# Optimization experiments

Hardware: AMD Instinct MI355X
Metric: run time of the kernel (lower is better)

Reference implementation:

```python
import jax, jax.numpy as jnp
import numpy as np

K = 4  # hard-coded in ParticleNet.__init__

# (fan_in, fan_out) for all linear layers
_DIMS = [(10, 32), (32, 64),        # edgeconv1 MLP (2*5 -> 32 -> 64)
         (128, 96), (96, 128),      # edgeconv2 MLP (2*64 -> 96 -> 128)
         (256, 192), (192, 256),    # edgeconv3 MLP (2*128 -> 192 -> 256)
         (453, 453), (453, 226), (226, 2)]  # output head (5+64+128+256=453)
_PNAMES = ['c1w1', 'c1w2', 'c2w1', 'c2w2', 'c3w1', 'c3w2', 'ow1', 'ow2', 'ow3']


def setup_inputs() -> dict:
    key = jax.random.key(0)
    ks = jax.random.split(key, 2 + len(_DIMS))
    inp = {
        'coords': jax.random.normal(ks[0], (1024, 128, 2), dtype=jnp.float32),
        'features': jax.random.normal(ks[1], (1024, 128, 5), dtype=jnp.float32),
    }
    for i, (name, (fi, fo)) in enumerate(zip(_PNAMES, _DIMS)):
        inp[name] = jax.random.normal(ks[2 + i], (fi, fo), dtype=jnp.float32) / np.sqrt(fi)
        inp[name.replace('w', 'b')] = jnp.zeros((fo,), dtype=jnp.float32)
    return inp


def _knn_idx(x, k):
    # x: [B,N,C] -> idx of k nearest neighbors (excluding self): [B,N,k]
    x2 = jnp.sum(x * x, axis=-1)                              # [B,N]
    d = x2[:, :, None] + x2[:, None, :] - 2.0 * jnp.einsum('bnc,bmc->bnm', x, x)
    d = d + jnp.eye(x.shape[1], dtype=x.dtype) * 1e9          # no self-loops
    _, idx = jax.lax.top_k(-d, k)
    return idx


def _edgeconv(x, idx, w1, b1, w2, b2):
    # EdgeConv: message = MLP([x_i, x_j - x_i]), mean-aggregated over k neighbors
    xj = jax.vmap(lambda xb, ib: xb[ib])(x, idx)              # [B,N,k,C]
    xi = jnp.broadcast_to(x[:, :, None, :], xj.shape)
    h = jnp.concatenate([xi, xj - xi], axis=-1)               # [B,N,k,2C]
    h = jax.nn.elu(h @ w1 + b1)
    h = jax.nn.elu(h @ w2 + b2)
    return jnp.mean(h, axis=2)                                # [B,N,out]


def reference(coords, features, c1w1, c1b1, c1w2, c1b2, c2w1, c2b1, c2w2, c2b2,
              c3w1, c3b1, c3w2, c3b2, ow1, ob1, ow2, ob2, ow3, ob3):
    idx1 = _knn_idx(coords, K)
    out1 = _edgeconv(features, idx1, c1w1, c1b1, c1w2, c1b2)  # [B,N,64]
    idx2 = _knn_idx(out1, K)
    out2 = _edgeconv(out1, idx2, c2w1, c2b1, c2w2, c2b2)      # [B,N,128]
    idx3 = _knn_idx(out2, K)
    out3 = _edgeconv(out2, idx3, c3w1, c3b1, c3w2, c3b2)      # [B,N,256]
    h = jnp.concatenate([features, out1, out2, out3], axis=-1)  # [B,N,453]
    h = jax.nn.elu(h @ ow1 + ob1)
    h = jax.nn.elu(h @ ow2 + ob2)
    return h @ ow3 + ob3                                      # [B,N,2]
```

## Files before the change

kernel.cpp:

```cpp
#include <hip/hip_runtime.h>
#include <cstdint>
#include <cstddef>


#define NB 1024
#define NPT 128

typedef __attribute__((ext_vector_type(8))) short short8;
typedef __attribute__((ext_vector_type(4))) float floatx4;
typedef __attribute__((ext_vector_type(4))) unsigned int uint4v;

__device__ __forceinline__ float elu_f(float x) { return x > 0.0f ? x : expm1f(x); }

__device__ __forceinline__ unsigned short f2bf(float f) {
  unsigned u = __builtin_bit_cast(unsigned, f);
  unsigned r = u + 0x7FFFu + ((u >> 16) & 1u);
  return (unsigned short)(r >> 16);
}
__device__ __forceinline__ float bf2f(unsigned short h) {
  unsigned u = ((unsigned)h) << 16;
  return __builtin_bit_cast(float, u);
}

template<int C>
__global__ __launch_bounds__(128) void knn_kernel(const float* __restrict__ x,
                                                  int* __restrict__ idx) {
  __shared__ __align__(16) float xs[NPT][C + 4];
  __shared__ float x2s[NPT];
  __shared__ double x2d[NPT];
  const int b = blockIdx.x, t = threadIdx.x;
  const float* xb = x + (size_t)b * NPT * C;
  for (int e = t; e < NPT * C; e += 128) xs[e / C][e % C] = xb[e];
  __syncthreads();
  float xi[C];
  float s2 = 0.0f;
  double s2d = 0.0;
#pragma unroll
  for (int c = 0; c < C; ++c) {
    xi[c] = xs[t][c];
    s2 += xi[c] * xi[c];
    s2d += (double)xi[c] * (double)xi[c];
  }
  x2s[t] = s2;
  x2d[t] = s2d;
  __syncthreads();
  float bd0 = 1e30f, bd1 = 1e30f, bd2 = 1e30f, bd3 = 1e30f, bd4 = 1e30f, bd5 = 1e30f;
  int bi0 = 0, bi1 = 0, bi2 = 0, bi3 = 0, bi4 = 0, bi5 = 0;
  for (int j = 0; j < NPT; ++j) {
    if (j == t) continue;
    float dot = 0.0f;
#pragma unroll
    for (int c = 0; c < C; ++c) dot += xi[c] * xs[j][c];
    float d = s2 + x2s[j] - 2.0f * dot;
    if (d < bd5) {
      bd5 = d; bi5 = j;
      if (bd5 < bd4) {
        float td = bd4; bd4 = bd5; bd5 = td; int ti = bi4; bi4 = bi5; bi5 = ti;
        if (bd4 < bd3) {
          td = bd3; bd3 = bd4; bd4 = td; ti = bi3; bi3 = bi4; bi4 = ti;
          if (bd3 < bd2) {
            td = bd2; bd2 = bd3; bd3 = td; ti = bi2; bi2 = bi3; bi3 = ti;
            if (bd2 < bd1) {
              td = bd1; bd1 = bd2; bd2 = td; ti = bi1; bi1 = bi2; bi2 = ti;
              if (bd1 < bd0) {
                td = bd0; bd0 = bd1; bd1 = td; ti = bi0; bi0 = bi1; bi1 = ti;
              }
            }
          }
        }
      }
    }
  }
  auto refine = [&](int j) -> double {
    double dot = 0.0;
#pragma unroll
    for (int c = 0; c < C; ++c) dot += (double)xi[c] * (double)xs[j][c];
    return s2d + x2d[j] - 2.0 * dot;
  };
  double e0 = refine(bi0), e1 = refine(bi1), e2 = refine(bi2);
  double e3 = refine(bi3), e4 = refine(bi4), e5 = refine(bi5);
#define CSWP(da, ia, db, ib)                                            \
  if ((da > db) || (da == db && ia > ib)) {                             \
    double _td = da; da = db; db = _td; int _ti = ia; ia = ib; ib = _ti; }
  CSWP(e0, bi0, e1, bi1) CSWP(e1, bi1, e2, bi2) CSWP(e2, bi2, e3, bi3)
  CSWP(e3, bi3, e4, bi4) CSWP(e4, bi4, e5, bi5)
  CSWP(e0, bi0, e1, bi1) CSWP(e1, bi1, e2, bi2) CSWP(e2, bi2, e3, bi3)
  CSWP(e3, bi3, e4, bi4)
  CSWP(e0, bi0, e1, bi1) CSWP(e1, bi1, e2, bi2) CSWP(e2, bi2, e3, bi3)
  CSWP(e0, bi0, e1, bi1) CSWP(e1, bi1, e2, bi2)
  CSWP(e0, bi0, e1, bi1)
#undef CSWP
  int* ib = idx + ((size_t)b * NPT + t) * 4;
  ib[0] = bi0; ib[1] = bi1; ib[2] = bi2; ib[3] = bi3;
}

template<int C>
__global__ __launch_bounds__(512) void knn512_kernel(const float* __restrict__ x,
                                                     int* __restrict__ idx) {
  constexpr int CQ = C / 4;
  constexpr int QS = CQ + 4;
  __shared__ __align__(16) float xs[NPT][4 * QS];
  __shared__ float x2s[NPT];
  __shared__ double x2d[NPT];
  const int b = blockIdx.x, t = threadIdx.x;
  const float* xb = x + (size_t)b * NPT * C;
  for (int e = t; e < NPT * C; e += 512) {
    int r = e / C, c = e % C;
    xs[r][(c / CQ) * QS + (c % CQ)] = xb[e];
  }
  __syncthreads();
  const int p = t >> 2, q = t & 3;
  float xi[CQ];
  float s2 = 0.f;
  double s2d = 0.0;
#pragma unroll
  for (int c = 0; c < CQ; ++c) {
    xi[c] = xs[p][q * QS + c];
    s2 += xi[c] * xi[c];
    s2d += (double)xi[c] * (double)xi[c];
  }
  s2 += __shfl_xor(s2, 1);  s2 += __shfl_xor(s2, 2);
  s2d += __shfl_xor(s2d, 1); s2d += __shfl_xor(s2d, 2);
  if (q == 0) { x2s[p] = s2; x2d[p] = s2d; }
  __syncthreads();
  float bd0 = 1e30f, bd1 = 1e30f, bd2 = 1e30f, bd3 = 1e30f, bd4 = 1e30f, bd5 = 1e30f;
  int bi0 = 0, bi1 = 0, bi2 = 0, bi3 = 0, bi4 = 0, bi5 = 0;
  for (int j = 0; j < NPT; ++j) {
    if (j == p) continue;
    const float4* xr = reinterpret_cast<const float4*>(&xs[j][q * QS]);
    float part0 = 0.f, part1 = 0.f, part2 = 0.f, part3 = 0.f;
#pragma unroll
    for (int c4 = 0; c4 < CQ / 4; ++c4) {
      float4 v = xr[c4];
      float s = xi[4 * c4 + 0] * v.x + xi[4 * c4 + 1] * v.y +
                xi[4 * c4 + 2] * v.z + xi[4 * c4 + 3] * v.w;
      if ((c4 & 3) == 0) part0 += s;
      else if ((c4 & 3) == 1) part1 += s;
      else if ((c4 & 3) == 2) part2 += s;
      else part3 += s;
    }
    float dot = (part0 + part1) + (part2 + part3);
    dot += __shfl_xor(dot, 1);
    dot += __shfl_xor(dot, 2);
    float d = s2 + x2s[j] - 2.0f * dot;
    if (d < bd5) {
      bd5 = d; bi5 = j;
      if (bd5 < bd4) {
        float td = bd4; bd4 = bd5; bd5 = td; int ti = bi4; bi4 = bi5; bi5 = ti;
        if (bd4 < bd3) {
          td = bd3; bd3 = bd4; bd4 = td; ti = bi3; bi3 = bi4; bi4 = ti;
          if (bd3 < bd2) {
            td = bd2; bd2 = bd3; bd3 = td; ti = bi2; bi2 = bi3; bi3 = ti;
            if (bd2 < bd1) {
              td = bd1; bd1 = bd2; bd2 = td; ti = bi1; bi1 = bi2; bi2 = ti;
              if (bd1 < bd0) {
                td = bd0; bd0 = bd1; bd1 = td; ti = bi0; bi0 = bi1; bi1 = ti;
              }
            }
          }
        }
      }
    }
  }
  auto refine = [&](int j) -> double {
    double dot = 0.0;
#pragma unroll
    for (int c = 0; c < CQ; ++c) dot += (double)xi[c] * (double)xs[j][q * QS + c];
    dot += __shfl_xor(dot, 1);
    dot += __shfl_xor(dot, 2);
    return s2d + x2d[j] - 2.0 * dot;
  };
  double e0 = refine(bi0), e1 = refine(bi1), e2 = refine(bi2);
  double e3 = refine(bi3), e4 = refine(bi4), e5 = refine(bi5);
#define CSWP(da, ia, db, ib)                                            \
  if ((da > db) || (da == db && ia > ib)) {                             \
    double _td = da; da = db; db = _td; int _ti = ia; ia = ib; ib = _ti; }
  CSWP(e0, bi0, e1, bi1) CSWP(e1, bi1, e2, bi2) CSWP(e2, bi2, e3, bi3)
  CSWP(e3, bi3, e4, bi4) CSWP(e4, bi4, e5, bi5)
  CSWP(e0, bi0, e1, bi1) CSWP(e1, bi1, e2, bi2) CSWP(e2, bi2, e3, bi3)
  CSWP(e3, bi3, e4, bi4)
  CSWP(e0, bi0, e1, bi1) CSWP(e1, bi1, e2, bi2) CSWP(e2, bi2, e3, bi3)
  CSWP(e0, bi0, e1, bi1) CSWP(e1, bi1, e2, bi2)
  CSWP(e0, bi0, e1, bi1)
#undef CSWP
  if (q == 0) {
    int* ib = idx + ((size_t)b * NPT + p) * 4;
    ib[0] = bi0; ib[1] = bi1; ib[2] = bi2; ib[3] = bi3;
  }
}

__global__ __launch_bounds__(256) void ec1_kernel(
    const float* __restrict__ feat, const int* __restrict__ idx,
    const float* __restrict__ w1, const float* __restrict__ b1,
    const float* __restrict__ w2, const float* __restrict__ b2,
    float* __restrict__ out) {
  __shared__ __align__(16) float fs[NPT][6];
  __shared__ __align__(16) float w1s[10][32];
  __shared__ __align__(16) float w2s[32][68];
  __shared__ float hs[256][33];
  __shared__ float b1s[32], b2s[64];
  const int z = blockIdx.x, t = threadIdx.x;
  const int b = z >> 1, hh = z & 1;
  const float* fb = feat + (size_t)b * NPT * 5;
  for (int e = t; e < NPT * 5; e += 256) fs[e / 5][e % 5] = fb[e];
  for (int e = t; e < 320; e += 256) w1s[e / 32][e % 32] = w1[e];
  for (int e = t; e < 2048; e += 256) w2s[e >> 6][e & 63] = w2[e];
  if (t < 32) b1s[t] = b1[t];
  if (t >= 192) b2s[t - 192] = b2[t - 192];
  __syncthreads();
  {
    const int p = hh * 64 + (t >> 2);
    const int j = idx[(size_t)b * 512 + p * 4 + (t & 3)];
    float h[32];
#pragma unroll
    for (int o = 0; o < 32; ++o) h[o] = b1s[o];
#pragma unroll
    for (int c = 0; c < 10; ++c) {
      float in_c = (c < 5) ? fs[p][c] : (fs[j][c - 5] - fs[p][c - 5]);
      const float4* wr = reinterpret_cast<const float4*>(&w1s[c][0]);
#pragma unroll
      for (int o4 = 0; o4 < 8; ++o4) {
        float4 w = wr[o4];
        h[4 * o4 + 0] += in_c * w.x; h[4 * o4 + 1] += in_c * w.y;
        h[4 * o4 + 2] += in_c * w.z; h[4 * o4 + 3] += in_c * w.w;
      }
    }
#pragma unroll
    for (int o = 0; o < 32; ++o) hs[t][o] = elu_f(h[o]);
  }
  __syncthreads();
  {
    const int g = t >> 2, q = t & 3;
    const int o0 = q * 16;
    float acc[4][16];
#pragma unroll
    for (int m = 0; m < 16; ++m) {
      float bv = b2s[o0 + m];
#pragma unroll
      for (int i = 0; i < 4; ++i) acc[i][m] = bv;
    }
    for (int k = 0; k < 32; ++k) {
      float hk0 = hs[g * 4 + 0][k];
      float hk1 = hs[g * 4 + 1][k];
      float hk2 = hs[g * 4 + 2][k];
      float hk3 = hs[g * 4 + 3][k];
      const float4* wr = reinterpret_cast<const float4*>(&w2s[k][o0]);
#pragma unroll
      for (int m4 = 0; m4 < 4; ++m4) {
        float4 w = wr[m4];
        acc[0][4 * m4 + 0] += hk0 * w.x; acc[0][4 * m4 + 1] += hk0 * w.y;
        acc[0][4 * m4 + 2] += hk0 * w.z; acc[0][4 * m4 + 3] += hk0 * w.w;
        acc[1][4 * m4 + 0] += hk1 * w.x; acc[1][4 * m4 + 1] += hk1 * w.y;
        acc[1][4 * m4 + 2] += hk1 * w.z; acc[1][4 * m4 + 3] += hk1 * w.w;
        acc[2][4 * m4 + 0] += hk2 * w.x; acc[2][4 * m4 + 1] += hk2 * w.y;
        acc[2][4 * m4 + 2] += hk2 * w.z; acc[2][4 * m4 + 3] += hk2 * w.w;
        acc[3][4 * m4 + 0] += hk3 * w.x; acc[3][4 * m4 + 1] += hk3 * w.y;
        acc[3][4 * m4 + 2] += hk3 * w.z; acc[3][4 * m4 + 3] += hk3 * w.w;
      }
    }
    float* ob = out + ((size_t)b * NPT + hh * 64 + g) * 64 + o0;
#pragma unroll
    for (int m4 = 0; m4 < 4; ++m4) {
      float4 v;
      float* vp = &v.x;
#pragma unroll
      for (int s = 0; s < 4; ++s) {
        int m = 4 * m4 + s;
        vp[s] = 0.25f * (elu_f(acc[0][m]) + elu_f(acc[1][m]) +
                         elu_f(acc[2][m]) + elu_f(acc[3][m]));
      }
      *reinterpret_cast<float4*>(&ob[4 * m4]) = v;
    }
  }
}

__global__ __launch_bounds__(512, 2) void ec2a_kernel(
    const float* __restrict__ x, const int* __restrict__ idx,
    const float* __restrict__ w1, const float* __restrict__ b1,
    float* __restrict__ H) {
  __shared__ __align__(16) float xs[NPT][68];
  __shared__ __align__(16) float w1s[128][100];
  __shared__ float b1s[96];
  const int b = blockIdx.x, t = threadIdx.x;
  const float* xb = x + (size_t)b * NPT * 64;
  for (int e = t; e < NPT * 64; e += 512) xs[e >> 6][e & 63] = xb[e];
  for (int e = t; e < 128 * 96; e += 512) w1s[e / 96][e % 96] = w1[e];
  if (t < 96) b1s[t] = b1[t];
  __syncthreads();
  const int pb = t >> 2, part = t & 3;
  const int n0 = part * 24;
  int jn[4];
#pragma unroll
  for (int i = 0; i < 4; ++i) jn[i] = idx[(size_t)b * 512 + pb * 4 + i];
  float acc[4][24];
#pragma unroll
  for (int m = 0; m < 24; ++m) {
    float bv = b1s[n0 + m];
#pragma unroll
    for (int i = 0; i < 4; ++i) acc[i][m] = bv;
  }
  for (int c = 0; c < 64; ++c) {
    float in_c = xs[pb][c];
    const float4* wr = reinterpret_cast<const float4*>(&w1s[c][n0]);
#pragma unroll
    for (int q4 = 0; q4 < 6; ++q4) {
      float4 wv = wr[q4];
#pragma unroll
      for (int i = 0; i < 4; ++i) {
        acc[i][4 * q4 + 0] += in_c * wv.x;
        acc[i][4 * q4 + 1] += in_c * wv.y;
        acc[i][4 * q4 + 2] += in_c * wv.z;
        acc[i][4 * q4 + 3] += in_c * wv.w;
      }
    }
  }
  for (int c = 0; c < 64; ++c) {
    float xic = xs[pb][c];
    float in0 = xs[jn[0]][c] - xic;
    float in1 = xs[jn[1]][c] - xic;
    float in2 = xs[jn[2]][c] - xic;
    float in3 = xs[jn[3]][c] - xic;
    const float4* wr = reinterpret_cast<const float4*>(&w1s[64 + c][n0]);
#pragma unroll
    for (int q4 = 0; q4 < 6; ++q4) {
      float4 wv = wr[q4];
      acc[0][4 * q4 + 0] += in0 * wv.x; acc[0][4 * q4 + 1] += in0 * wv.y;
      acc[0][4 * q4 + 2] += in0 * wv.z; acc[0][4 * q4 + 3] += in0 * wv.w;
      acc[1][4 * q4 + 0] += in1 * wv.x; acc[1][4 * q4 + 1] += in1 * wv.y;
      acc[1][4 * q4 + 2] += in1 * wv.z; acc[1][4 * q4 + 3] += in1 * wv.w;
      acc[2][4 * q4 + 0] += in2 * wv.x; acc[2][4 * q4 + 1] += in2 * wv.y;
      acc[2][4 * q4 + 2] += in2 * wv.z; acc[2][4 * q4 + 3] += in2 * wv.w;
      acc[3][4 * q4 + 0] += in3 * wv.x; acc[3][4 * q4 + 1] += in3 * wv.y;
      acc[3][4 * q4 + 2] += in3 * wv.z; acc[3][4 * q4 + 3] += in3 * wv.w;
    }
  }
#pragma unroll
  for (int i = 0; i < 4; ++i) {
    float* hrow = H + ((size_t)b * 512 + pb * 4 + i) * 96 + n0;
#pragma unroll
    for (int q4 = 0; q4 < 6; ++q4) {
      float4 v = {elu_f(acc[i][4 * q4 + 0]), elu_f(acc[i][4 * q4 + 1]),
                  elu_f(acc[i][4 * q4 + 2]), elu_f(acc[i][4 * q4 + 3])};
      *reinterpret_cast<float4*>(&hrow[4 * q4]) = v;
    }
  }
}

__global__ __launch_bounds__(512, 2) void ec2b_kernel(
    const float* __restrict__ H, const float* __restrict__ w2,
    const float* __restrict__ b2, float* __restrict__ out) {
  __shared__ __align__(16) float hsT[96][260];
  __shared__ float w2s[96][132];
  __shared__ float b2s[128];
  const int z = blockIdx.x, t = threadIdx.x;
  const int bc = z >> 1, hh = z & 1;
  const float* Hb = H + ((size_t)bc * 512 + hh * 256) * 96;
  for (int i = t; i < 256 * 96; i += 512) hsT[i % 96][i / 96] = Hb[i];
  for (int i = t; i < 96 * 128; i += 512) w2s[i >> 7][i & 127] = w2[i];
  if (t < 128) b2s[t] = b2[t];
  __syncthreads();
  const int g = t >> 3, oq = t & 7;
  float acc[4][16];
#pragma unroll
  for (int m = 0; m < 16; ++m) {
    float bv = b2s[oq + 8 * m];
#pragma unroll
    for (int i = 0; i < 4; ++i) acc[i][m] = bv;
  }
  for (int k = 0; k < 96; ++k) {
    float4 hv = *reinterpret_cast<const float4*>(&hsT[k][4 * g]);
#pragma unroll
    for (int m = 0; m < 16; ++m) {
      float wv = w2s[k][oq + 8 * m];
      acc[0][m] += hv.x * wv;
      acc[1][m] += hv.y * wv;
      acc[2][m] += hv.z * wv;
      acc[3][m] += hv.w * wv;
    }
  }
  float* orow = out + ((size_t)bc * NPT + hh * 64 + g) * 128;
#pragma unroll
  for (int m = 0; m < 16; ++m) {
    float s = elu_f(acc[0][m]) + elu_f(acc[1][m]) +
              elu_f(acc[2][m]) + elu_f(acc[3][m]);
    orow[oq + 8 * m] = 0.25f * s;
  }
}

__global__ __launch_bounds__(512, 2) void ec3a_kernel(
    const float* __restrict__ x, const int* __restrict__ idx,
    const unsigned short* __restrict__ w1t3g, const float* __restrict__ b1,
    unsigned short* __restrict__ h1) {
  __shared__ unsigned short Xb[128][136];
  __shared__ __align__(16) unsigned short W1t[192][264];
  __shared__ float b1s[192];
  __shared__ unsigned short stg[8][16][40];
  const int b = blockIdx.x, t = threadIdx.x;
  const float* xb = x + (size_t)b * NPT * 128;
  for (int e = t; e < NPT * 128; e += 512) Xb[e >> 7][e & 127] = f2bf(xb[e]);
  {
    const uint4v* src = reinterpret_cast<const uint4v*>(w1t3g);
    uint4v* dst = reinterpret_cast<uint4v*>(&W1t[0][0]);
    for (int i = t; i < 192 * 264 / 8; i += 512) dst[i] = src[i];
  }
  if (t < 192) b1s[t] = b1[t];
  __syncthreads();
  const int w = t >> 6, l = t & 63;
  const int lr = l & 15, lq = l >> 4;
  for (int mt = 0; mt < 4; ++mt) {
    const int m = (w * 4 + mt) * 16;
    const int e = m + lr;
    const int p = e >> 2;
    const int jp = idx[(size_t)b * 512 + e];
    short8 A[8];
#pragma unroll
    for (int kk = 0; kk < 4; ++kk) {
      int k0 = kk * 32 + lq * 8;
      A[kk] = *reinterpret_cast<const short8*>(&Xb[p][k0]);
    }
#pragma unroll
    for (int kk = 0; kk < 4; ++kk) {
      int k0 = kk * 32 + lq * 8;
      short8 aj = *reinterpret_cast<const short8*>(&Xb[jp][k0]);
      short8 ai = *reinterpret_cast<const short8*>(&Xb[p][k0]);
      short8 d;
#pragma unroll
      for (int q = 0; q < 8; ++q)
        d[q] = (short)f2bf(bf2f((unsigned short)aj[q]) - bf2f((unsigned short)ai[q]));
      A[4 + kk] = d;
    }
    floatx4 acc[12];
#pragma unroll
    for (int n = 0; n < 12; ++n) acc[n] = (floatx4){0.f, 0.f, 0.f, 0.f};
#pragma unroll
    for (int n = 0; n < 12; ++n) {
#pragma unroll
      for (int kk = 0; kk < 8; ++kk) {
        short8 Bf = *reinterpret_cast<const short8*>(&W1t[n * 16 + lr][kk * 32 + lq * 8]);
        acc[n] = __builtin_amdgcn_mfma_f32_16x16x32_bf16(A[kk], Bf, acc[n], 0, 0, 0);
      }
    }
#pragma unroll
    for (int pr = 0; pr < 6; ++pr) {
      float bv0 = b1s[pr * 32 + lr];
      float bv1 = b1s[pr * 32 + 16 + lr];
#pragma unroll
      for (int i = 0; i < 4; ++i) {
        stg[w][lq * 4 + i][lr]      = f2bf(elu_f(acc[2 * pr][i] + bv0));
        stg[w][lq * 4 + i][16 + lr] = f2bf(elu_f(acc[2 * pr + 1][i] + bv1));
      }
      asm volatile("s_waitcnt lgkmcnt(0)" ::: "memory");
      const unsigned short* src = &stg[w][l >> 2][(l & 3) * 8];
      uint4v vv = *reinterpret_cast<const uint4v*>(src);
      size_t dst = ((size_t)b * 512 + m + (l >> 2)) * 192 + pr * 32 + (l & 3) * 8;
      *reinterpret_cast<uint4v*>(&h1[dst]) = vv;
      asm volatile("s_waitcnt lgkmcnt(0)" ::: "memory");
    }
  }
}

__global__ __launch_bounds__(512, 2) void ec3b_kernel(
    const unsigned short* __restrict__ h1,
    const unsigned short* __restrict__ w2t3g, const float* __restrict__ b2,
    unsigned short* __restrict__ out3) {
  __shared__ __align__(16) unsigned short W2t[256][200];
  __shared__ float b2s[256];
  const int b = blockIdx.x, t = threadIdx.x;
  {
    const uint4v* src = reinterpret_cast<const uint4v*>(w2t3g);
    uint4v* dst = reinterpret_cast<uint4v*>(&W2t[0][0]);
    for (int i = t; i < 256 * 200 / 8; i += 512) dst[i] = src[i];
  }
  if (t < 256) b2s[t] = b2[t];
  __syncthreads();
  const int w = t >> 6, l = t & 63;
  const int lr = l & 15, lq = l >> 4;
  for (int mt = 0; mt < 4; ++mt) {
    const int m = (w * 4 + mt) * 16;
    floatx4 acc[16];
#pragma unroll
    for (int n = 0; n < 16; ++n) acc[n] = (floatx4){0.f, 0.f, 0.f, 0.f};
    const unsigned short* arow = h1 + ((size_t)b * 512 + m + lr) * 192;
#pragma unroll
    for (int kk = 0; kk < 6; ++kk) {
      short8 Af = *reinterpret_cast<const short8*>(&arow[kk * 32 + lq * 8]);
#pragma unroll
      for (int n = 0; n < 16; ++n) {
        short8 Bf = *reinterpret_cast<const short8*>(&W2t[n * 16 + lr][kk * 32 + lq * 8]);
        acc[n] = __builtin_amdgcn_mfma_f32_16x16x32_bf16(Af, Bf, acc[n], 0, 0, 0);
      }
    }
    unsigned short* orow = out3 + ((size_t)b * NPT + (m >> 2) + lq) * 256;
#pragma unroll
    for (int n = 0; n < 16; ++n) {
      float bv = b2s[n * 16 + lr];
      float s = 0.f;
#pragma unroll
      for (int i = 0; i < 4; ++i) s += elu_f(acc[n][i] + bv);
      orow[n * 16 + lr] = f2bf(0.25f * s);
    }
  }
}

__global__ __launch_bounds__(256) void prep_kernel(
    const float* __restrict__ hw1, const float* __restrict__ hw2,
    const float* __restrict__ c3w1, const float* __restrict__ c3w2,
    unsigned short* __restrict__ w1p, unsigned short* __restrict__ w2p,
    unsigned short* __restrict__ w1t3g, unsigned short* __restrict__ w2t3g) {
  int i = blockIdx.x * 256 + threadIdx.x;
  if (i < 512 * 480) {
    int n = i / 480, kp = i % 480;
    int ko = (kp < 5) ? kp : kp - 3;
    bool ok = ((kp < 5) || (kp >= 8 && kp < 456)) && (n < 453);
    w1p[i] = ok ? f2bf(hw1[(size_t)ko * 453 + n]) : (unsigned short)0;
  } else if (i < 512 * 480 + 256 * 480) {
    int j = i - 512 * 480;
    int n = j / 480, kp = j % 480;
    bool ok = (kp < 453) && (n < 226);
    w2p[j] = ok ? f2bf(hw2[(size_t)kp * 226 + n]) : (unsigned short)0;
  } else if (i < 512 * 480 + 256 * 480 + 192 * 264) {
    int m = i - (512 * 480 + 256 * 480);
    int n = m / 264, k = m % 264;
    w1t3g[m] = (k < 256) ? f2bf(c3w1[(size_t)k * 192 + n]) : (unsigned short)0;
  } else {
    int m = i - (512 * 480 + 256 * 480 + 192 * 264);
    if (m < 256 * 200) {
      int n = m / 200, k = m % 200;
      w2t3g[m] = (k < 192) ? f2bf(c3w2[(size_t)k * 256 + n]) : (unsigned short)0;
    }
  }
}

#define HSTR 488
#define TPSS 72
__global__ __launch_bounds__(256, 2) void head_mfma_kernel(
    const float* __restrict__ feat, const float* __restrict__ o1,
    const float* __restrict__ o2, const unsigned short* __restrict__ o3,
    const unsigned short* __restrict__ w1p, const float* __restrict__ b1,
    const unsigned short* __restrict__ w2p, const float* __restrict__ b2,
    const float* __restrict__ w3, const float* __restrict__ b3,
    float* __restrict__ out) {
  __shared__ unsigned short uA[64 * HSTR];
  __shared__ __align__(16) unsigned short tps[4][16][TPSS];
  __shared__ float b1s[512], b2s[256], w3s[512];
  const int t = threadIdx.x;
  const size_t base = (size_t)blockIdx.x * 64;

  for (int i = t; i < 512; i += 256) b1s[i] = (i < 453) ? b1[i] : 0.f;
  if (t < 256) b2s[t] = (t < 226) ? b2[t] : 0.f;
  for (int i = t; i < 512; i += 256) w3s[i] = (i < 452) ? w3[i] : 0.f;

  const int w = t >> 6, l = t & 63;
  const int lr = l & 15, lq = l >> 4;
  const int tr = t >> 2, tc = t & 3;
  const size_t grow = base + w * 16 + lr;

  short8 Af[15];
#pragma unroll
  for (int kk = 0; kk < 15; ++kk) {
    const int kbase = kk * 32 + lq * 8;
    short8 r;
    if (kbase >= 456) {
#pragma unroll
      for (int q = 0; q < 8; ++q) r[q] = 0;
    } else if (kbase >= 200) {
      r = *reinterpret_cast<const short8*>(&o3[grow * 256 + (kbase - 200)]);
    } else if (kbase >= 72) {
      const float* s = &o2[grow * 128 + (kbase - 72)];
#pragma unroll
      for (int q = 0; q < 8; ++q) r[q] = (short)f2bf(s[q]);
    } else if (kbase >= 8) {
      const float* s = &o1[grow * 64 + (kbase - 8)];
#pragma unroll
      for (int q = 0; q < 8; ++q) r[q] = (short)f2bf(s[q]);
    } else {
      const float* s = &feat[grow * 5];
#pragma unroll
      for (int q = 0; q < 8; ++q) r[q] = (q < 5) ? (short)f2bf(s[q]) : (short)0;
    }
    Af[kk] = r;
  }

  uint4v v[15];
#define WLOAD(SRC, CH)                                                   \
  {                                                                      \
    _Pragma("unroll")                                                    \
    for (int i = 0; i < 15; ++i)                                         \
      v[i] = *reinterpret_cast<const uint4v*>(                           \
          &SRC[((size_t)((CH) * 64 + tr)) * 480 + (tc + 4 * i) * 8]);    \
  }
#define WWRITE()                                                         \
  {                                                                      \
    _Pragma("unroll")                                                    \
    for (int i = 0; i < 15; ++i)                                         \
      *reinterpret_cast<uint4v*>(&uA[tr * HSTR + (tc + 4 * i) * 8]) = v[i]; \
  }

  WLOAD(w1p, 0)
  WWRITE()
  __syncthreads();

  short8 Af2[15];
#pragma unroll
  for (int ch = 0; ch < 8; ++ch) {
    if (ch < 7) WLOAD(w1p, ch + 1)
    else       WLOAD(w2p, 0)
    floatx4 a0 = {0.f, 0.f, 0.f, 0.f}, a1 = {0.f, 0.f, 0.f, 0.f};
    floatx4 a2 = {0.f, 0.f, 0.f, 0.f}, a3 = {0.f, 0.f, 0.f, 0.f};
#pragma unroll
    for (int kk = 0; kk < 15; ++kk) {
      int ko = kk * 32 + lq * 8;
      short8 B0 = *reinterpret_cast<const short8*>(&uA[(lr)*HSTR + ko]);
      short8 B1 = *reinterpret_cast<const short8*>(&uA[(16 + lr) * HSTR + ko]);
      short8 B2 = *reinterpret_cast<const short8*>(&uA[(32 + lr) * HSTR + ko]);
      short8 B3 = *reinterpret_cast<const short8*>(&uA[(48 + lr) * HSTR + ko]);
      a0 = __builtin_amdgcn_mfma_f32_16x16x32_bf16(Af[kk], B0, a0, 0, 0, 0);
      a1 = __builtin_amdgcn_mfma_f32_16x16x32_bf16(Af[kk], B1, a1, 0, 0, 0);
      a2 = __builtin_amdgcn_mfma_f32_16x16x32_bf16(Af[kk], B2, a2, 0, 0, 0);
      a3 = __builtin_amdgcn_mfma_f32_16x16x32_bf16(Af[kk], B3, a3, 0, 0, 0);
    }
    {
      floatx4 aj[4] = {a0, a1, a2, a3};
#pragma unroll
      for (int jx = 0; jx < 4; ++jx) {
        int c = ch * 64 + jx * 16 + lr;
        float bb = b1s[c];
#pragma unroll
        for (int i = 0; i < 4; ++i)
          tps[w][lq * 4 + i][jx * 16 + lr] = f2bf(elu_f(aj[jx][i] + bb));
      }
    }
    asm volatile("s_waitcnt lgkmcnt(0)" ::: "memory");
    Af2[2 * ch] = *reinterpret_cast<const short8*>(&tps[w][lr][lq * 8]);
    if (ch < 7)
      Af2[2 * ch + 1] = *reinterpret_cast<const short8*>(&tps[w][lr][32 + lq * 8]);
    asm volatile("s_waitcnt lgkmcnt(0)" ::: "memory");
    __syncthreads();
    WWRITE()
    __syncthreads();
  }

  float p0[4] = {0.f, 0.f, 0.f, 0.f}, p1[4] = {0.f, 0.f, 0.f, 0.f};
#pragma unroll
  for (int ch = 0; ch < 4; ++ch) {
    if (ch < 3) WLOAD(w2p, ch + 1)
    floatx4 a0 = {0.f, 0.f, 0.f, 0.f}, a1 = {0.f, 0.f, 0.f, 0.f};
    floatx4 a2 = {0.f, 0.f, 0.f, 0.f}, a3 = {0.f, 0.f, 0.f, 0.f};
#pragma unroll
    for (int kk = 0; kk < 15; ++kk) {
      int ko = kk * 32 + lq * 8;
      short8 B0 = *reinterpret_cast<const short8*>(&uA[(lr)*HSTR + ko]);
      short8 B1 = *reinterpret_cast<const short8*>(&uA[(16 + lr) * HSTR + ko]);
      short8 B2 = *reinterpret_cast<const short8*>(&uA[(32 + lr) * HSTR + ko]);
      short8 B3 = *reinterpret_cast<const short8*>(&uA[(48 + lr) * HSTR + ko]);
      a0 = __builtin_amdgcn_mfma_f32_16x16x32_bf16(Af2[kk], B0, a0, 0, 0, 0);
      a1 = __builtin_amdgcn_mfma_f32_16x16x32_bf16(Af2[kk], B1, a1, 0, 0, 0);
      a2 = __builtin_amdgcn_mfma_f32_16x16x32_bf16(Af2[kk], B2, a2, 0, 0, 0);
      a3 = __builtin_amdgcn_mfma_f32_16x16x32_bf16(Af2[kk], B3, a3, 0, 0, 0);
    }
    {
      floatx4 aj[4] = {a0, a1, a2, a3};
#pragma unroll
      for (int jx = 0; jx < 4; ++jx) {
        int c = ch * 64 + jx * 16 + lr;
        float bb = b2s[c];
        float wa = w3s[2 * c], wb = w3s[2 * c + 1];
#pragma unroll
        for (int i = 0; i < 4; ++i) {
          float h = (c < 226) ? elu_f(aj[jx][i] + bb) : 0.f;
          p0[i] += h * wa;
          p1[i] += h * wb;
        }
      }
    }
    if (ch < 3) {
      __syncthreads();
      WWRITE()
      __syncthreads();
    }
  }

#pragma unroll
  for (int i = 0; i < 4; ++i) {
    float a = p0[i], bvv = p1[i];
#pragma unroll
    for (int m = 1; m < 16; m <<= 1) {
      a += __shfl_xor(a, m);
      bvv += __shfl_xor(bvv, m);
    }
    if (lr == 0) {
      size_t row = base + w * 16 + lq * 4 + i;
      float2 vv = {a + b3[0], bvv + b3[1]};
      *reinterpret_cast<float2*>(&out[row * 2]) = vv;
    }
  }
#undef WLOAD
#undef WWRITE
}

extern "C" void kernel_launch(void* const* d_in, const int* in_sizes, int n_in,
                              void* d_out, int out_size, void* d_ws, size_t ws_size,
                              hipStream_t stream) {
  const float* coords = (const float*)d_in[0];
  const float* feat   = (const float*)d_in[1];
  const float* c1w1 = (const float*)d_in[2];  const float* c1b1 = (const float*)d_in[3];
  const float* c1w2 = (const float*)d_in[4];  const float* c1b2 = (const float*)d_in[5];
  const float* c2w1 = (const float*)d_in[6];  const float* c2b1 = (const float*)d_in[7];
  const float* c2w2 = (const float*)d_in[8];  const float* c2b2 = (const float*)d_in[9];
  const float* c3w1 = (const float*)d_in[10]; const float* c3b1 = (const float*)d_in[11];
  const float* c3w2 = (const float*)d_in[12]; const float* c3b2 = (const float*)d_in[13];
  const float* ow1  = (const float*)d_in[14]; const float* ob1  = (const float*)d_in[15];
  const float* ow2  = (const float*)d_in[16]; const float* ob2  = (const float*)d_in[17];
  const float* ow3  = (const float*)d_in[18]; const float* ob3  = (const float*)d_in[19];
  float* out = (float*)d_out;

  char* ws = (char*)d_ws;
  float* out1 = (float*)(ws);
  float* out2 = (float*)(ws + (32ull << 20));
  unsigned short* out3b = (unsigned short*)(ws + (96ull << 20));
  float* Hbuf2 = (float*)(ws + (96ull << 20));
  unsigned short* h1 = (unsigned short*)(ws + (162ull << 20));
  unsigned short* w1p = (unsigned short*)(ws + (212ull << 20));
  unsigned short* w2p = (unsigned short*)(ws + (212ull << 20) + (512ull << 10));
  unsigned short* w1t3g = (unsigned short*)(ws + (213ull << 20));
  unsigned short* w2t3g = (unsigned short*)(ws + (213ull << 20) + (256ull << 10));
  int* idx = (int*)(ws + (214ull << 20));

  prep_kernel<<<1838, 256, 0, stream>>>(ow1, ow2, c3w1, c3w2,
                                        w1p, w2p, w1t3g, w2t3g);
  knn_kernel<2><<<NB, 128, 0, stream>>>(coords, idx);
  ec1_kernel<<<2 * NB, 256, 0, stream>>>(feat, idx, c1w1, c1b1, c1w2, c1b2, out1);
  knn512_kernel<64><<<NB, 512, 0, stream>>>(out1, idx);
  for (int c = 0; c < 2; ++c) {
    ec2a_kernel<<<512, 512, 0, stream>>>(out1 + (size_t)c * 512 * NPT * 64,
                                         idx + (size_t)c * 512 * 512,
                                         c2w1, c2b1, Hbuf2);
    ec2b_kernel<<<1024, 512, 0, stream>>>(Hbuf2, c2w2, c2b2,
                                          out2 + (size_t)c * 512 * NPT * 128);
  }
  knn512_kernel<128><<<NB, 512, 0, stream>>>(out2, idx);
  for (int c = 0; c < 4; ++c) {
    ec3a_kernel<<<256, 512, 0, stream>>>(out2 + (size_t)c * 256 * NPT * 128,
                                         idx + (size_t)c * 256 * 512,
                                         w1t3g, c3b1, h1);
    ec3b_kernel<<<256, 512, 0, stream>>>(h1, w2t3g, c3b2,
                                         out3b + (size_t)c * 256 * NPT * 256);
  }
  head_mfma_kernel<<<2048, 256, 0, stream>>>(feat, out1, out2, out3b,
                                             w1p, ob1, w2p, ob2, ow3, ob3, out);
}
```

Before: 1.981 ms.

## Compute kNN distance matrices with split-bf16 MFMA instead of scalar FP32 dots

Replaces the scalar per-thread dot-product kNN for the 64- and 128-channel layers with a kernel that computes the Gram matrix on MFMA bf16 units. Each value is split into hi and lo bf16 parts, and three products are summed to approximate FP32 accuracy. Each lane keeps a partial top-6 over its rows, and the partial lists are merged across lane groups with shuffles. The candidates are then refined in double precision from an FP32 copy reloaded into the same LDS buffer. This removes the large scalar FMA and LDS traffic of the pairwise distances, at the cost of extra LDS staging, a second global load, and a small risk of neighbour-ordering differences near ties.

Result: faster. 1.729 ms, median of 3 (-12.7%).

```diff
diff --git a/kernel.cpp b/kernel.cpp
--- a/kernel.cpp
+++ b/kernel.cpp
@@ -21,6 +21,21 @@
   unsigned u = ((unsigned)h) << 16;
   return __builtin_bit_cast(float, u);
 }
+
+#define INS6(dv, jv)                                                    \
+  if ((dv) < bd5) {                                                     \
+    bd5 = (dv); bi5 = (jv);                                             \
+    if (bd5 < bd4) {                                                    \
+      float _t = bd4; bd4 = bd5; bd5 = _t; int _i = bi4; bi4 = bi5; bi5 = _i; \
+      if (bd4 < bd3) {                                                  \
+        _t = bd3; bd3 = bd4; bd4 = _t; _i = bi3; bi3 = bi4; bi4 = _i;   \
+        if (bd3 < bd2) {                                                \
+          _t = bd2; bd2 = bd3; bd3 = _t; _i = bi2; bi2 = bi3; bi3 = _i; \
+          if (bd2 < bd1) {                                              \
+            _t = bd1; bd1 = bd2; bd2 = _t; _i = bi1; bi1 = bi2; bi2 = _i; \
+            if (bd1 < bd0) {                                            \
+              _t = bd0; bd0 = bd1; bd1 = _t; _i = bi0; bi0 = bi1; bi1 = _i; \
+            } } } } } }
 
 template<int C>
 __global__ __launch_bounds__(128) void knn_kernel(const float* __restrict__ x,
@@ -52,24 +67,7 @@
 #pragma unroll
     for (int c = 0; c < C; ++c) dot += xi[c] * xs[j][c];
     float d = s2 + x2s[j] - 2.0f * dot;
-    if (d < bd5) {
-      bd5 = d; bi5 = j;
-      if (bd5 < bd4) {
-        float td = bd4; bd4 = bd5; bd5 = td; int ti = bi4; bi4 = bi5; bi5 = ti;
-        if (bd4 < bd3) {
-          td = bd3; bd3 = bd4; bd4 = td; ti = bi3; bi3 = bi4; bi4 = ti;
-          if (bd3 < bd2) {
-            td = bd2; bd2 = bd3; bd3 = td; ti = bi2; bi2 = bi3; bi3 = ti;
-            if (bd2 < bd1) {
-              td = bd1; bd1 = bd2; bd2 = td; ti = bi1; bi1 = bi2; bi2 = ti;
-              if (bd1 < bd0) {
-                td = bd0; bd0 = bd1; bd1 = td; ti = bi0; bi0 = bi1; bi1 = ti;
-              }
-            }
-          }
-        }
-      }
-    }
+    INS6(d, j)
   }
   auto refine = [&](int j) -> double {
     double dot = 0.0;
@@ -95,80 +93,108 @@
 }
 
 template<int C>
-__global__ __launch_bounds__(512) void knn512_kernel(const float* __restrict__ x,
-                                                     int* __restrict__ idx) {
+__global__ __launch_bounds__(512) void knn_mfma_kernel(const float* __restrict__ x,
+                                                       int* __restrict__ idx) {
+  constexpr int KC = C / 32;
+  constexpr int HS = C + 8;
+  constexpr int FS = C + 4;
   constexpr int CQ = C / 4;
-  constexpr int QS = CQ + 4;
-  __shared__ __align__(16) float xs[NPT][4 * QS];
+  __shared__ __align__(16) unsigned short lbuf[2 * NPT * HS];
   __shared__ float x2s[NPT];
   __shared__ double x2d[NPT];
+  unsigned short* Xhi = lbuf;
+  unsigned short* Xlo = lbuf + NPT * HS;
+  float* Xs = reinterpret_cast<float*>(lbuf);
   const int b = blockIdx.x, t = threadIdx.x;
   const float* xb = x + (size_t)b * NPT * C;
   for (int e = t; e < NPT * C; e += 512) {
     int r = e / C, c = e % C;
-    xs[r][(c / CQ) * QS + (c % CQ)] = xb[e];
-  }
-  __syncthreads();
-  const int p = t >> 2, q = t & 3;
-  float xi[CQ];
-  float s2 = 0.f;
-  double s2d = 0.0;
-#pragma unroll
-  for (int c = 0; c < CQ; ++c) {
-    xi[c] = xs[p][q * QS + c];
-    s2 += xi[c] * xi[c];
-    s2d += (double)xi[c] * (double)xi[c];
-  }
-  s2 += __shfl_xor(s2, 1);  s2 += __shfl_xor(s2, 2);
-  s2d += __shfl_xor(s2d, 1); s2d += __shfl_xor(s2d, 2);
-  if (q == 0) { x2s[p] = s2; x2d[p] = s2d; }
-  __syncthreads();
+    float v = xb[e];
+    unsigned short h = f2bf(v);
+    Xhi[r * HS + c] = h;
+    Xlo[r * HS + c] = f2bf(v - bf2f(h));
+  }
+  {
+    const int p = t >> 2, q = t & 3;
+    const float4* r4 = reinterpret_cast<const float4*>(xb + p * C + q * CQ);
+    float s2 = 0.f;
+    double s2d = 0.0;
+#pragma unroll
+    for (int c4 = 0; c4 < CQ / 4; ++c4) {
+      float4 v = r4[c4];
+      s2 += v.x * v.x + v.y * v.y + v.z * v.z + v.w * v.w;
+      s2d += (double)v.x * v.x + (double)v.y * v.y +
+             (double)v.z * v.z + (double)v.w * v.w;
+    }
+    s2 += __shfl_xor(s2, 1);  s2 += __shfl_xor(s2, 2);
+    s2d += __shfl_xor(s2d, 1); s2d += __shfl_xor(s2d, 2);
+    if (q == 0) { x2s[p] = s2; x2d[p] = s2d; }
+  }
+  __syncthreads();
+  const int w = t >> 6, l = t & 63;
+  const int lr = l & 15, lq = l >> 4;
+  const int iq = w * 16 + lr;
+  short8 Bhi[KC], Blo[KC];
+#pragma unroll
+  for (int kk = 0; kk < KC; ++kk) {
+    Bhi[kk] = *reinterpret_cast<const short8*>(&Xhi[iq * HS + kk * 32 + lq * 8]);
+    Blo[kk] = *reinterpret_cast<const short8*>(&Xlo[iq * HS + kk * 32 + lq * 8]);
+  }
+  const float x2i = x2s[iq];
   float bd0 = 1e30f, bd1 = 1e30f, bd2 = 1e30f, bd3 = 1e30f, bd4 = 1e30f, bd5 = 1e30f;
   int bi0 = 0, bi1 = 0, bi2 = 0, bi3 = 0, bi4 = 0, bi5 = 0;
-  for (int j = 0; j < NPT; ++j) {
-    if (j == p) continue;
-    const float4* xr = reinterpret_cast<const float4*>(&xs[j][q * QS]);
-    float part0 = 0.f, part1 = 0.f, part2 = 0.f, part3 = 0.f;
-#pragma unroll
-    for (int c4 = 0; c4 < CQ / 4; ++c4) {
-      float4 v = xr[c4];
-      float s = xi[4 * c4 + 0] * v.x + xi[4 * c4 + 1] * v.y +
-                xi[4 * c4 + 2] * v.z + xi[4 * c4 + 3] * v.w;
-      if ((c4 & 3) == 0) part0 += s;
-      else if ((c4 & 3) == 1) part1 += s;
-      else if ((c4 & 3) == 2) part2 += s;
-      else part3 += s;
-    }
-    float dot = (part0 + part1) + (part2 + part3);
-    dot += __shfl_xor(dot, 1);
-    dot += __shfl_xor(dot, 2);
-    float d = s2 + x2s[j] - 2.0f * dot;
-    if (d < bd5) {
-      bd5 = d; bi5 = j;
-      if (bd5 < bd4) {
-        float td = bd4; bd4 = bd5; bd5 = td; int ti = bi4; bi4 = bi5; bi5 = ti;
-        if (bd4 < bd3) {
-          td = bd3; bd3 = bd4; bd4 = td; ti = bi3; bi3 = bi4; bi4 = ti;
-          if (bd3 < bd2) {
-            td = bd2; bd2 = bd3; bd3 = td; ti = bi2; bi2 = bi3; bi3 = ti;
-            if (bd2 < bd1) {
-              td = bd1; bd1 = bd2; bd2 = td; ti = bi1; bi1 = bi2; bi2 = ti;
-              if (bd1 < bd0) {
-                td = bd0; bd0 = bd1; bd1 = td; ti = bi0; bi0 = bi1; bi1 = ti;
-              }
-            }
-          }
-        }
-      }
-    }
-  }
+#pragma unroll
+  for (int jt = 0; jt < 8; ++jt) {
+    short8 Ahi[KC], Alo[KC];
+#pragma unroll
+    for (int kk = 0; kk < KC; ++kk) {
+      Ahi[kk] = *reinterpret_cast<const short8*>(
+          &Xhi[(jt * 16 + lr) * HS + kk * 32 + lq * 8]);
+      Alo[kk] = *reinterpret_cast<const short8*>(
+          &Xlo[(jt * 16 + lr) * HS + kk * 32 + lq * 8]);
+    }
+    floatx4 g = {0.f, 0.f, 0.f, 0.f};
+#pragma unroll
+    for (int kk = 0; kk < KC; ++kk) {
+      g = __builtin_amdgcn_mfma_f32_16x16x32_bf16(Ahi[kk], Bhi[kk], g, 0, 0, 0);
+      g = __builtin_amdgcn_mfma_f32_16x16x32_bf16(Ahi[kk], Blo[kk], g, 0, 0, 0);
+      g = __builtin_amdgcn_mfma_f32_16x16x32_bf16(Alo[kk], Bhi[kk], g, 0, 0, 0);
+    }
+#pragma unroll
+    for (int r = 0; r < 4; ++r) {
+      int j = jt * 16 + lq * 4 + r;
+      float d = (j == iq) ? 1e30f : (x2i + x2s[j] - 2.0f * g[r]);
+      INS6(d, j)
+    }
+  }
+#pragma unroll
+  for (int rnd = 0; rnd < 2; ++rnd) {
+    const int m = 16 << rnd;
+    float od0 = __shfl_xor(bd0, m), od1 = __shfl_xor(bd1, m), od2 = __shfl_xor(bd2, m);
+    float od3 = __shfl_xor(bd3, m), od4 = __shfl_xor(bd4, m), od5 = __shfl_xor(bd5, m);
+    int oi0 = __shfl_xor(bi0, m), oi1 = __shfl_xor(bi1, m), oi2 = __shfl_xor(bi2, m);
+    int oi3 = __shfl_xor(bi3, m), oi4 = __shfl_xor(bi4, m), oi5 = __shfl_xor(bi5, m);
+    INS6(od0, oi0) INS6(od1, oi1) INS6(od2, oi2)
+    INS6(od3, oi3) INS6(od4, oi4) INS6(od5, oi5)
+  }
+  bi0 = __shfl(bi0, lr); bi1 = __shfl(bi1, lr); bi2 = __shfl(bi2, lr);
+  bi3 = __shfl(bi3, lr); bi4 = __shfl(bi4, lr); bi5 = __shfl(bi5, lr);
+  __syncthreads();
+  for (int e = t; e < NPT * C; e += 512) {
+    int r = e / C, c = e % C;
+    Xs[r * FS + c] = xb[e];
+  }
+  __syncthreads();
+  const double x2di = x2d[iq];
   auto refine = [&](int j) -> double {
     double dot = 0.0;
-#pragma unroll
-    for (int c = 0; c < CQ; ++c) dot += (double)xi[c] * (double)xs[j][q * QS + c];
-    dot += __shfl_xor(dot, 1);
-    dot += __shfl_xor(dot, 2);
-    return s2d + x2d[j] - 2.0 * dot;
+    const float* ri = &Xs[iq * FS + lq * CQ];
+    const float* rj = &Xs[j * FS + lq * CQ];
+#pragma unroll
+    for (int c = 0; c < CQ; ++c) dot += (double)ri[c] * (double)rj[c];
+    dot += __shfl_xor(dot, 16);
+    dot += __shfl_xor(dot, 32);
+    return x2di + x2d[j] - 2.0 * dot;
   };
   double e0 = refine(bi0), e1 = refine(bi1), e2 = refine(bi2);
   double e3 = refine(bi3), e4 = refine(bi4), e5 = refine(bi5);
@@ -183,8 +209,8 @@
   CSWP(e0, bi0, e1, bi1) CSWP(e1, bi1, e2, bi2)
   CSWP(e0, bi0, e1, bi1)
 #undef CSWP
-  if (q == 0) {
-    int* ib = idx + ((size_t)b * NPT + p) * 4;
+  if (lq == 0) {
+    int* ib = idx + ((size_t)b * NPT + iq) * 4;
     ib[0] = bi0; ib[1] = bi1; ib[2] = bi2; ib[3] = bi3;
   }
 }
@@ -730,7 +756,7 @@
                                         w1p, w2p, w1t3g, w2t3g);
   knn_kernel<2><<<NB, 128, 0, stream>>>(coords, idx);
   ec1_kernel<<<2 * NB, 256, 0, stream>>>(feat, idx, c1w1, c1b1, c1w2, c1b2, out1);
-  knn512_kernel<64><<<NB, 512, 0, stream>>>(out1, idx);
+  knn_mfma_kernel<64><<<NB, 512, 0, stream>>>(out1, idx);
   for (int c = 0; c < 2; ++c) {
     ec2a_kernel<<<512, 512, 0, stream>>>(out1 + (size_t)c * 512 * NPT * 64,
                                          idx + (size_t)c * 512 * 512,
@@ -738,7 +764,7 @@
     ec2b_kernel<<<1024, 512, 0, stream>>>(Hbuf2, c2w2, c2b2,
                                           out2 + (size_t)c * 512 * NPT * 128);
   }
-  knn512_kernel<128><<<NB, 512, 0, stream>>>(out2, idx);
+  knn_mfma_kernel<128><<<NB, 512, 0, stream>>>(out2, idx);
   for (int c = 0; c < 4; ++c) {
     ec3a_kernel<<<256, 512, 0, stream>>>(out2 + (size_t)c * 256 * NPT * 128,
                                          idx + (size_t)c * 256 * 512,
```
